# Kernel tuning notes

Measured on AMD Instinct MI355X. Metric: run time of the kernel, lower is better.

Reference implementation:

```python
import jax, jax.numpy as jnp
import numpy as np

D = 256  # feature_dim
B, N = 16, 1024
NEG_SLOPE = 0.2
SCALE = float(np.sqrt(D))


def setup_inputs() -> dict:
    key = jax.random.key(0)
    ks = jax.random.split(key, 8)
    s = 1.0 / np.sqrt(D)  # torch Linear default init scale
    return {
        "feature": jax.random.normal(ks[0], (B, N, D), dtype=jnp.float32),
        "graph": jax.random.randint(ks[1], (B, N, N), 0, 2, dtype=jnp.int32),
        "W_w": jax.random.uniform(ks[2], (D, D), jnp.float32, -s, s),
        "W_b": jax.random.uniform(ks[3], (D,), jnp.float32, -s, s),
        "Q_w": jax.random.uniform(ks[4], (D, D), jnp.float32, -s, s),
        "Q_b": jax.random.uniform(ks[5], (D,), jnp.float32, -s, s),
        "K_w": jax.random.uniform(ks[6], (D, D), jnp.float32, -s, s),
        "K_b": jax.random.uniform(ks[7], (D,), jnp.float32, -s, s),
    }


def reference(feature, graph, W_w, W_b, Q_w, Q_b, K_w, K_b):
    # h = W(feature); torch Linear: x @ W.T + b
    h = jnp.einsum('bnd,ed->bne', feature, W_w) + W_b        # [B,N,D]
    q = jnp.einsum('bnd,ed->bne', h, Q_w) + Q_b              # [B,N,D]
    k = jnp.einsum('bnd,ed->bne', h, K_w) + K_b              # [B,N,D]
    e = jnp.einsum('bnd,bmd->bnm', q, k) / SCALE             # [B,N,N]
    e = jnp.where(e >= 0, e, NEG_SLOPE * e)                  # LeakyReLU(0.2)
    e = jnp.where(graph == 0, jnp.float32(-1e9), e)          # mask
    a = jax.nn.softmax(e, axis=2)                            # dropout = identity (eval)
    out = jax.nn.relu(jnp.einsum('bnm,bmd->bnd', a, h))      # [B,N,D]
    return out
```

## Files before the change

### kernel.cpp

```cpp
#include <hip/hip_runtime.h>
#include <hip/hip_bf16.h>
#include <stdint.h>

#define DD 256
#define NB 16
#define NN 1024
#define MTOT (NB * NN)

typedef __attribute__((ext_vector_type(8))) short short8;
typedef __attribute__((ext_vector_type(4))) float f32x4;

__device__ __forceinline__ ushort f2b(float f) {
  uint32_t u = __float_as_uint(f);
  return (ushort)((u + 0x7fffu + ((u >> 16) & 1u)) >> 16);
}

template <bool A_F32, bool WRITE_T>
__global__ __launch_bounds__(256, 1) void gemm_hqk(
    const void* __restrict__ Aptr, const float* __restrict__ W,
    const float* __restrict__ bias, ushort* __restrict__ C,
    ushort* __restrict__ CT) {
  __shared__ ushort Wl[256 * 256];
  const int tid = threadIdx.x;

  for (int i = 0; i < 64; ++i) {
    int idx4 = i * 256 + tid;
    int row = idx4 >> 6;
    int col0 = (idx4 & 63) << 2;
    float4 v = ((const float4*)W)[idx4];
    ushort4 b4;
    b4.x = f2b(v.x); b4.y = f2b(v.y); b4.z = f2b(v.z); b4.w = f2b(v.w);
    int byte = (row * 512 + col0 * 2) ^ ((row & 7) << 4);
    *(ushort4*)((char*)Wl + byte) = b4;
  }
  __syncthreads();

  const int w = tid >> 6, lane = tid & 63, l15 = lane & 15, hi = lane >> 4;
  const int m0 = blockIdx.x * 64 + w * 16;
  const int arow = m0 + l15;

  f32x4 acc[16] = {};

#pragma unroll
  for (int kk = 0; kk < 8; ++kk) {
    const int k0 = kk * 32 + hi * 8;
    short8 a;
    if constexpr (A_F32) {
      const float4* ap = (const float4*)((const float*)Aptr + arow * 256 + k0);
      float4 x = ap[0], y = ap[1];
      a[0] = (short)f2b(x.x); a[1] = (short)f2b(x.y);
      a[2] = (short)f2b(x.z); a[3] = (short)f2b(x.w);
      a[4] = (short)f2b(y.x); a[5] = (short)f2b(y.y);
      a[6] = (short)f2b(y.z); a[7] = (short)f2b(y.w);
    } else {
      a = *(const short8*)((const ushort*)Aptr + arow * 256 + k0);
    }
#pragma unroll
    for (int et = 0; et < 16; ++et) {
      int er = et * 16 + l15;
      short8 bf = *(const short8*)((const char*)Wl +
                                   ((er * 512 + k0 * 2) ^ ((er & 7) << 4)));
      acc[et] = __builtin_amdgcn_mfma_f32_16x16x32_bf16(a, bf, acc[et], 0, 0, 0);
    }
  }

  ushort hvals[16][4];
#pragma unroll
  for (int et = 0; et < 16; ++et) {
    int e = et * 16 + l15;
    float bv = bias[e];
#pragma unroll
    for (int r = 0; r < 4; ++r) {
      ushort hb = f2b(acc[et][r] + bv);
      hvals[et][r] = hb;
      C[(m0 + hi * 4 + r) * 256 + e] = hb;
    }
  }

  if constexpr (WRITE_T) {
    __syncthreads();
    ushort* Tl = Wl;
    const int mloc = w * 16 + hi * 4;
#pragma unroll
    for (int et = 0; et < 16; ++et)
#pragma unroll
      for (int r = 0; r < 4; ++r)
        Tl[(et * 16 + l15) * 64 + mloc + r] = hvals[et][r];
    __syncthreads();
    const int bidx = blockIdx.x >> 4;
    const int n0 = (blockIdx.x & 15) * 64;
    ushort* dst = CT + bidx * (256 * 1024) + tid * 1024 + n0;
    const uint4* src = (const uint4*)(Tl + tid * 64);
#pragma unroll
    for (int j = 0; j < 8; ++j) ((uint4*)dst)[j] = src[j];
  }
}

__global__ __launch_bounds__(256, 1) void gemm_qk(
    const ushort* __restrict__ h, const float* __restrict__ Qw,
    const float* __restrict__ Qb, const float* __restrict__ Kw,
    const float* __restrict__ Kb_, ushort* __restrict__ q,
    ushort* __restrict__ k) {
  __shared__ ushort Wl[256 * 256];
  const int tid = threadIdx.x;
  const bool isK = blockIdx.x >= 256;
  const float* W = isK ? Kw : Qw;
  const float* bias = isK ? Kb_ : Qb;
  ushort* C = isK ? k : q;
  const int bid = blockIdx.x & 255;

  for (int i = 0; i < 64; ++i) {
    int idx4 = i * 256 + tid;
    int row = idx4 >> 6;
    int col0 = (idx4 & 63) << 2;
    float4 v = ((const float4*)W)[idx4];
    ushort4 b4;
    b4.x = f2b(v.x); b4.y = f2b(v.y); b4.z = f2b(v.z); b4.w = f2b(v.w);
    int byte = (row * 512 + col0 * 2) ^ ((row & 7) << 4);
    *(ushort4*)((char*)Wl + byte) = b4;
  }
  __syncthreads();

  const int w = tid >> 6, lane = tid & 63, l15 = lane & 15, hi = lane >> 4;
  const int m0 = bid * 64 + w * 16;
  const int arow = m0 + l15;

  f32x4 acc[16] = {};

#pragma unroll
  for (int kk = 0; kk < 8; ++kk) {
    const int k0 = kk * 32 + hi * 8;
    short8 a = *(const short8*)(h + arow * 256 + k0);
#pragma unroll
    for (int et = 0; et < 16; ++et) {
      int er = et * 16 + l15;
      short8 bf = *(const short8*)((const char*)Wl +
                                   ((er * 512 + k0 * 2) ^ ((er & 7) << 4)));
      acc[et] = __builtin_amdgcn_mfma_f32_16x16x32_bf16(a, bf, acc[et], 0, 0, 0);
    }
  }

#pragma unroll
  for (int et = 0; et < 16; ++et) {
    int e = et * 16 + l15;
    float bv = bias[e];
#pragma unroll
    for (int r = 0; r < 4; ++r)
      C[(m0 + hi * 4 + r) * 256 + e] = f2b(acc[et][r] + bv);
  }
}

#define SM_KT 0
#define SM_HT 32768
#define SM_PL 65536
#define SM_M2 73728
#define SM_CM 74752
#define SM_SZ 75008

__device__ __forceinline__ int pswz(int row, int bytecol) {
  return (row * 64 + bytecol) ^ ((row & 7) << 4) ^ ((row >> 3) << 5);
}

__global__ __launch_bounds__(512, 2) void attn8(
    const ushort* __restrict__ Q, const ushort* __restrict__ Kb,
    const ushort* __restrict__ HT, const int* __restrict__ graph,
    float* __restrict__ out) {
  __shared__ __align__(16) char smem[SM_SZ];
  ushort* Kt = (ushort*)(smem + SM_KT);
  ushort* Ht = (ushort*)(smem + SM_HT);
  ushort* Pl = (ushort*)(smem + SM_PL);
  uint* M2 = (uint*)(smem + SM_M2);
  float* Cm = (float*)(smem + SM_CM);

  const int tid = threadIdx.x;
  const int w = tid >> 6, lane = tid & 63, l15 = lane & 15, hi = lane >> 4;
  const int wg = w >> 1, half = w & 1;
  const int hw = blockIdx.x;
  const int slot = hw >> 3;
  const int b = (hw & 7) * 2 + (slot >> 4);
  const int q0 = (slot & 15) * 64;
  const int qrow_a = q0 + wg * 16 + l15;
  const int qrow_cl = wg * 16 + hi * 4;
  const int* grow_base = graph + (b * 1024 + q0 + w * 8) * 1024 + lane;

  int greg[8];

#pragma unroll
  for (int j = 0; j < 8; ++j) greg[j] = grow_base[j * 1024];

  short8 qf[8];
#pragma unroll
  for (int kk = 0; kk < 8; ++kk)
    qf[kk] = *(const short8*)(Q + (b * 1024 + qrow_a) * 256 + kk * 32 + hi * 8);

#pragma unroll
  for (int j = 0; j < 8; ++j) {
    unsigned long long mm = __ballot(greg[j] != 0);
    if (lane == 0) {
      M2[(w * 8 + j) * 2] = (uint)mm;
      M2[(w * 8 + j) * 2 + 1] = (uint)(mm >> 32);
    }
  }

  float lR[4] = {0.f, 0.f, 0.f, 0.f};
  f32x4 o[16] = {};

  for (int t = 0; t < 16; ++t) {
    const uint* M2c = M2 + (t & 1) * 128;
    uint* M2n = M2 + ((t & 1) ^ 1) * 128;

    __syncthreads();
#pragma unroll
    for (int i = 0; i < 4; ++i) {
      int c = i * 512 + tid;
      int krow = c >> 5, col0 = (c & 31) << 3;
      uint4 v = *(const uint4*)(Kb + (b * 1024 + t * 64 + krow) * 256 + col0);
      *(uint4*)((char*)Kt + ((krow * 512 + col0 * 2) ^ ((krow & 7) << 4))) = v;
    }
#pragma unroll
    for (int i = 0; i < 4; ++i) {
      int c = i * 512 + tid;
      int drow = c >> 3, col0 = (c & 7) << 3;
      uint4 v = *(const uint4*)(HT + b * (256 * 1024) + drow * 1024 + t * 64 + col0);
      *(uint4*)((char*)Ht + ((drow * 128 + col0 * 2) ^ ((drow & 7) << 4))) = v;
    }
    __syncthreads();

    if (t < 15) {
#pragma unroll
      for (int j = 0; j < 8; ++j) greg[j] = grow_base[j * 1024 + (t + 1) * 64];
    }

    f32x4 s[2] = {};
    __builtin_amdgcn_s_setprio(1);
#pragma unroll
    for (int kk = 0; kk < 8; ++kk) {
#pragma unroll
      for (int nt = 0; nt < 2; ++nt) {
        int krow = half * 32 + nt * 16 + l15;
        short8 kf = *(const short8*)((const char*)Kt +
            ((krow * 512 + (kk * 32 + hi * 8) * 2) ^ ((krow & 7) << 4)));
        s[nt] = __builtin_amdgcn_mfma_f32_16x16x32_bf16(qf[kk], kf, s[nt], 0, 0, 0);
      }
    }
    __builtin_amdgcn_s_setprio(0);

    float p[2][4];
#pragma unroll
    for (int r = 0; r < 4; ++r) {
      uint mw = M2c[(qrow_cl + r) * 2 + half];
      float v0 = s[0][r] * 0.0625f; v0 = (v0 >= 0.f) ? v0 : 0.2f * v0;
      float v1 = s[1][r] * 0.0625f; v1 = (v1 >= 0.f) ? v1 : 0.2f * v1;
      float p0 = ((mw >> l15) & 1u) ? __expf(v0) : 0.f;
      float p1 = ((mw >> (16 + l15)) & 1u) ? __expf(v1) : 0.f;
      p[0][r] = p0; p[1][r] = p1;
      lR[r] += p0 + p1;
    }

    ushort* Pw = Pl + w * 512;
#pragma unroll
    for (int nt = 0; nt < 2; ++nt)
#pragma unroll
      for (int r = 0; r < 4; ++r) {
        int row = hi * 4 + r, col = nt * 16 + l15;
        *(ushort*)((char*)Pw + pswz(row, col * 2)) = f2b(p[nt][r]);
      }
    __asm__ volatile("s_waitcnt lgkmcnt(0)" ::: "memory");
    short8 pa = *(const short8*)((const char*)Pw + pswz(l15, hi * 16));

    __builtin_amdgcn_s_setprio(1);
#pragma unroll
    for (int dt = 0; dt < 16; ++dt) {
      int dcol = dt * 16 + l15;
      short8 hf = *(const short8*)((const char*)Ht +
          ((dcol * 128 + (half * 32 + hi * 8) * 2) ^ ((dcol & 7) << 4)));
      o[dt] = __builtin_amdgcn_mfma_f32_16x16x32_bf16(pa, hf, o[dt], 0, 0, 0);
    }
    __builtin_amdgcn_s_setprio(0);

    if (t < 15) {
#pragma unroll
      for (int j = 0; j < 8; ++j) {
        unsigned long long mm = __ballot(greg[j] != 0);
        if (lane == 0) {
          M2n[(w * 8 + j) * 2] = (uint)mm;
          M2n[(w * 8 + j) * 2 + 1] = (uint)(mm >> 32);
        }
      }
    }
  }

#pragma unroll
  for (int r = 0; r < 4; ++r) {
    lR[r] += __shfl_xor(lR[r], 1);
    lR[r] += __shfl_xor(lR[r], 2);
    lR[r] += __shfl_xor(lR[r], 4);
    lR[r] += __shfl_xor(lR[r], 8);
  }

  __syncthreads();
  float* Ob = (float*)smem;
  if (half == 1) {
#pragma unroll
    for (int dt = 0; dt < 16; ++dt)
#pragma unroll
      for (int r = 0; r < 4; ++r) {
        int row = hi * 4 + r;
        int byte = (row * 1024 + (dt * 16 + l15) * 4) ^ ((row & 15) << 6);
        *(float*)((char*)Ob + wg * 16384 + byte) = o[dt][r];
      }
    if (l15 == 0) {
#pragma unroll
      for (int r = 0; r < 4; ++r)
        Cm[wg * 16 + hi * 4 + r] = lR[r];
    }
  }
  __syncthreads();
  if (half == 0) {
#pragma unroll
    for (int r = 0; r < 4; ++r) {
      int rowl = hi * 4 + r;
      float inv = 1.f / (lR[r] + Cm[wg * 16 + rowl]);
      int orow = b * 1024 + q0 + wg * 16 + rowl;
#pragma unroll
      for (int dt = 0; dt < 16; ++dt) {
        int byte = (rowl * 1024 + (dt * 16 + l15) * 4) ^ ((rowl & 15) << 6);
        float ob = *(const float*)((const char*)Ob + wg * 16384 + byte);
        float v = (o[dt][r] + ob) * inv;
        out[orow * 256 + dt * 16 + l15] = fmaxf(v, 0.f);
      }
    }
  }
}

extern "C" void kernel_launch(void* const* d_in, const int* in_sizes, int n_in,
                              void* d_out, int out_size, void* d_ws,
                              size_t ws_size, hipStream_t stream) {
  const float* feature = (const float*)d_in[0];
  const int* graph = (const int*)d_in[1];
  const float* W_w = (const float*)d_in[2];
  const float* W_b = (const float*)d_in[3];
  const float* Q_w = (const float*)d_in[4];
  const float* Q_b = (const float*)d_in[5];
  const float* K_w = (const float*)d_in[6];
  const float* K_b = (const float*)d_in[7];
  float* out = (float*)d_out;

  ushort* h = (ushort*)d_ws;
  ushort* hT = h + MTOT * DD;
  ushort* q = hT + MTOT * DD;
  ushort* k = q + MTOT * DD;

  gemm_hqk<true, true><<<256, 256, 0, stream>>>(feature, W_w, W_b, h, hT);
  gemm_qk<<<512, 256, 0, stream>>>(h, Q_w, Q_b, K_w, K_b, q, k);
  attn8<<<256, 512, 0, stream>>>(q, k, hT, graph, out);
}
```

Measured before the change: 97.31 us.

## Fuse h, q, k projection GEMMs into one kernel reusing h from LDS

Merges the h projection kernel and the q/k projection kernel into a single kernel. Each block keeps its 64-row h tile in LDS, builds the MFMA A operands from it in registers, then restages the Q and K weights in turn to compute q and k. This drops one launch and the global write and re-read of row-major h. The cost is that each block serially stages three weight matrices and q and k run sequentially within a block, using 256 blocks instead of 512 for the q/k work, which lowers parallelism.

```diff
diff --git a/kernel.cpp b/kernel.cpp
--- a/kernel.cpp
+++ b/kernel.cpp
@@ -15,14 +15,8 @@
   return (ushort)((u + 0x7fffu + ((u >> 16) & 1u)) >> 16);
 }
 
-template <bool A_F32, bool WRITE_T>
-__global__ __launch_bounds__(256, 1) void gemm_hqk(
-    const void* __restrict__ Aptr, const float* __restrict__ W,
-    const float* __restrict__ bias, ushort* __restrict__ C,
-    ushort* __restrict__ CT) {
-  __shared__ ushort Wl[256 * 256];
-  const int tid = threadIdx.x;
-
+__device__ __forceinline__ void stage_weights(const float* __restrict__ W,
+                                              ushort* Wl, int tid) {
   for (int i = 0; i < 64; ++i) {
     int idx4 = i * 256 + tid;
     int row = idx4 >> 6;
@@ -33,28 +27,34 @@
     int byte = (row * 512 + col0 * 2) ^ ((row & 7) << 4);
     *(ushort4*)((char*)Wl + byte) = b4;
   }
-  __syncthreads();
-
+}
+
+__global__ __launch_bounds__(256, 1) void gemm_fused(
+    const float* __restrict__ feature, const float* __restrict__ W_w,
+    const float* __restrict__ W_b, const float* __restrict__ Q_w,
+    const float* __restrict__ Q_b, const float* __restrict__ K_w,
+    const float* __restrict__ K_b, ushort* __restrict__ hT,
+    ushort* __restrict__ q, ushort* __restrict__ k) {
+  __shared__ ushort Wl[256 * 256];
+  const int tid = threadIdx.x;
   const int w = tid >> 6, lane = tid & 63, l15 = lane & 15, hi = lane >> 4;
   const int m0 = blockIdx.x * 64 + w * 16;
   const int arow = m0 + l15;
 
+  stage_weights(W_w, Wl, tid);
+  __syncthreads();
+
   f32x4 acc[16] = {};
-
 #pragma unroll
   for (int kk = 0; kk < 8; ++kk) {
     const int k0 = kk * 32 + hi * 8;
+    const float4* ap = (const float4*)(feature + arow * 256 + k0);
+    float4 x = ap[0], y = ap[1];
     short8 a;
-    if constexpr (A_F32) {
-      const float4* ap = (const float4*)((const float*)Aptr + arow * 256 + k0);
-      float4 x = ap[0], y = ap[1];
-      a[0] = (short)f2b(x.x); a[1] = (short)f2b(x.y);
-      a[2] = (short)f2b(x.z); a[3] = (short)f2b(x.w);
-      a[4] = (short)f2b(y.x); a[5] = (short)f2b(y.y);
-      a[6] = (short)f2b(y.z); a[7] = (short)f2b(y.w);
-    } else {
-      a = *(const short8*)((const ushort*)Aptr + arow * 256 + k0);
-    }
+    a[0] = (short)f2b(x.x); a[1] = (short)f2b(x.y);
+    a[2] = (short)f2b(x.z); a[3] = (short)f2b(x.w);
+    a[4] = (short)f2b(y.x); a[5] = (short)f2b(y.y);
+    a[6] = (short)f2b(y.z); a[7] = (short)f2b(y.w);
 #pragma unroll
     for (int et = 0; et < 16; ++et) {
       int er = et * 16 + l15;
@@ -67,86 +67,88 @@
   ushort hvals[16][4];
 #pragma unroll
   for (int et = 0; et < 16; ++et) {
-    int e = et * 16 + l15;
-    float bv = bias[e];
-#pragma unroll
-    for (int r = 0; r < 4; ++r) {
-      ushort hb = f2b(acc[et][r] + bv);
-      hvals[et][r] = hb;
-      C[(m0 + hi * 4 + r) * 256 + e] = hb;
-    }
-  }
-
-  if constexpr (WRITE_T) {
-    __syncthreads();
-    ushort* Tl = Wl;
+    float bv = W_b[et * 16 + l15];
+#pragma unroll
+    for (int r = 0; r < 4; ++r) hvals[et][r] = f2b(acc[et][r] + bv);
+  }
+
+  __syncthreads();
+  ushort* Tl = Wl;
+  {
     const int mloc = w * 16 + hi * 4;
 #pragma unroll
     for (int et = 0; et < 16; ++et)
 #pragma unroll
       for (int r = 0; r < 4; ++r)
         Tl[(et * 16 + l15) * 64 + mloc + r] = hvals[et][r];
-    __syncthreads();
+  }
+  __syncthreads();
+
+  short8 qa[8];
+#pragma unroll
+  for (int kk = 0; kk < 8; ++kk) {
+    const int k0 = kk * 32 + hi * 8;
+#pragma unroll
+    for (int j = 0; j < 8; ++j)
+      qa[kk][j] = (short)Tl[(k0 + j) * 64 + w * 16 + l15];
+  }
+  {
     const int bidx = blockIdx.x >> 4;
     const int n0 = (blockIdx.x & 15) * 64;
-    ushort* dst = CT + bidx * (256 * 1024) + tid * 1024 + n0;
+    ushort* dst = hT + bidx * (256 * 1024) + tid * 1024 + n0;
     const uint4* src = (const uint4*)(Tl + tid * 64);
 #pragma unroll
     for (int j = 0; j < 8; ++j) ((uint4*)dst)[j] = src[j];
   }
-}
-
-__global__ __launch_bounds__(256, 1) void gemm_qk(
-    const ushort* __restrict__ h, const float* __restrict__ Qw,
-    const float* __restrict__ Qb, const float* __restrict__ Kw,
-    const float* __restrict__ Kb_, ushort* __restrict__ q,
-    ushort* __restrict__ k) {
-  __shared__ ushort Wl[256 * 256];
-  const int tid = threadIdx.x;
-  const bool isK = blockIdx.x >= 256;
-  const float* W = isK ? Kw : Qw;
-  const float* bias = isK ? Kb_ : Qb;
-  ushort* C = isK ? k : q;
-  const int bid = blockIdx.x & 255;
-
-  for (int i = 0; i < 64; ++i) {
-    int idx4 = i * 256 + tid;
-    int row = idx4 >> 6;
-    int col0 = (idx4 & 63) << 2;
-    float4 v = ((const float4*)W)[idx4];
-    ushort4 b4;
-    b4.x = f2b(v.x); b4.y = f2b(v.y); b4.z = f2b(v.z); b4.w = f2b(v.w);
-    int byte = (row * 512 + col0 * 2) ^ ((row & 7) << 4);
-    *(ushort4*)((char*)Wl + byte) = b4;
-  }
-  __syncthreads();
-
-  const int w = tid >> 6, lane = tid & 63, l15 = lane & 15, hi = lane >> 4;
-  const int m0 = bid * 64 + w * 16;
-  const int arow = m0 + l15;
-
-  f32x4 acc[16] = {};
-
+  __syncthreads();
+
+  stage_weights(Q_w, Wl, tid);
+  __syncthreads();
+#pragma unroll
+  for (int et = 0; et < 16; ++et) acc[et] = (f32x4){0.f, 0.f, 0.f, 0.f};
 #pragma unroll
   for (int kk = 0; kk < 8; ++kk) {
     const int k0 = kk * 32 + hi * 8;
-    short8 a = *(const short8*)(h + arow * 256 + k0);
 #pragma unroll
     for (int et = 0; et < 16; ++et) {
       int er = et * 16 + l15;
       short8 bf = *(const short8*)((const char*)Wl +
                                    ((er * 512 + k0 * 2) ^ ((er & 7) << 4)));
-      acc[et] = __builtin_amdgcn_mfma_f32_16x16x32_bf16(a, bf, acc[et], 0, 0, 0);
-    }
-  }
-
+      acc[et] = __builtin_amdgcn_mfma_f32_16x16x32_bf16(qa[kk], bf, acc[et], 0, 0, 0);
+    }
+  }
 #pragma unroll
   for (int et = 0; et < 16; ++et) {
     int e = et * 16 + l15;
-    float bv = bias[e];
+    float bv = Q_b[e];
 #pragma unroll
     for (int r = 0; r < 4; ++r)
-      C[(m0 + hi * 4 + r) * 256 + e] = f2b(acc[et][r] + bv);
+      q[(m0 + hi * 4 + r) * 256 + e] = f2b(acc[et][r] + bv);
+  }
+  __syncthreads();
+
+  stage_weights(K_w, Wl, tid);
+  __syncthreads();
+#pragma unroll
+  for (int et = 0; et < 16; ++et) acc[et] = (f32x4){0.f, 0.f, 0.f, 0.f};
+#pragma unroll
+  for (int kk = 0; kk < 8; ++kk) {
+    const int k0 = kk * 32 + hi * 8;
+#pragma unroll
+    for (int et = 0; et < 16; ++et) {
+      int er = et * 16 + l15;
+      short8 bf = *(const short8*)((const char*)Wl +
+                                   ((er * 512 + k0 * 2) ^ ((er & 7) << 4)));
+      acc[et] = __builtin_amdgcn_mfma_f32_16x16x32_bf16(qa[kk], bf, acc[et], 0, 0, 0);
+    }
+  }
+#pragma unroll
+  for (int et = 0; et < 16; ++et) {
+    int e = et * 16 + l15;
+    float bv = K_b[e];
+#pragma unroll
+    for (int r = 0; r < 4; ++r)
+      k[(m0 + hi * 4 + r) * 256 + e] = f2b(acc[et][r] + bv);
   }
 }
 
@@ -346,12 +348,11 @@
   const float* K_b = (const float*)d_in[7];
   float* out = (float*)d_out;
 
-  ushort* h = (ushort*)d_ws;
-  ushort* hT = h + MTOT * DD;
+  ushort* hT = (ushort*)d_ws;
   ushort* q = hT + MTOT * DD;
   ushort* k = q + MTOT * DD;
 
-  gemm_hqk<true, true><<<256, 256, 0, stream>>>(feature, W_w, W_b, h, hT);
-  gemm_qk<<<512, 256, 0, stream>>>(h, Q_w, Q_b, K_w, K_b, q, k);
+  gemm_fused<<<256, 256, 0, stream>>>(feature, W_w, W_b, Q_w, Q_b, K_w, K_b,
+                                      hT, q, k);
   attn8<<<256, 512, 0, stream>>>(q, k, hT, graph, out);
 }
```

Result: faster. 93.69 us (median of 2 runs) (-3.7%).
